# Performance work log

Hardware: AMD Instinct MI355X
Metric: run time of the kernel (lower is better)

The kernel has to match this reference:

```python
import jax, jax.numpy as jnp
import numpy as np

N, D = 8192, 32
SIGMA = 4.0
DAMPING = 0.5
MAX_ITER = 10
SHIFT_TOL = 1e-4


def _sqdist(a, b):
    # squared euclidean distances, (Na, Nb)
    sq = jnp.sum(a * a, axis=1)[:, None] + jnp.sum(b * b, axis=1)[None, :] - 2.0 * (a @ b.T)
    return jnp.maximum(sq, 0.0)


def setup_inputs() -> dict:
    key = jax.random.key(0)
    x = jax.random.normal(key, (N, D), dtype=jnp.float32)
    sigma = jnp.asarray(SIGMA, dtype=jnp.float32)  # learned scalar nn.Parameter
    return {"x": x, "sigma": sigma}


def _find_centroids(x, sigma):
    gamma = 1.0 / (2.0 * sigma ** 2)

    def body(carry, _):
        centroids, done = carry
        sq = _sqdist(x, centroids)              # (N, N); cdist(x,c)**2
        w = jnp.exp(-sq * gamma)                # gaussian kernel weights
        new_c = (w @ x) / jnp.sum(w, axis=1, keepdims=True)
        shift = jnp.linalg.norm(new_c - centroids, axis=1)
        # torch breaks BEFORE the damping update when max shift < tol
        done_new = done | (jnp.max(shift) < SHIFT_TOL)
        centroids = jnp.where(done_new, centroids,
                              DAMPING * centroids + (1.0 - DAMPING) * new_c)
        return (centroids, done_new), None

    (centroids, _), _ = jax.lax.scan(jax.remat(body), (x, jnp.asarray(False)), None, length=MAX_ITER)
    return centroids


def _nms_keep(x, centroids, threshold):
    n = centroids.shape[0]
    sq_pc = _sqdist(x, centroids)
    closest = jnp.argmin(sq_pc, axis=1)                      # (N,)
    scores = jnp.zeros((n,), jnp.int32).at[closest].add(1)   # counts per centroid
    sq_cc = _sqdist(centroids, centroids)
    overlap = (sq_cc < threshold ** 2) & ~jnp.eye(n, dtype=bool)
    order = jnp.argsort(-scores)                             # descending by score

    def body(keep, idx):
        active = keep[idx]
        keep2 = jnp.where(active, keep & ~overlap[idx], keep)
        keep2 = keep2.at[idx].set(jnp.where(active, scores[idx] > 0, keep2[idx]))
        return keep2, None

    keep, _ = jax.lax.scan(body, jnp.ones((n,), bool), order)
    return keep


def reference(x, sigma):
    centroids = _find_centroids(x, sigma)
    # threshold = sigma.item() in torch -> constant w.r.t. autodiff
    keep = _nms_keep(x, centroids, jax.lax.stop_gradient(sigma))
    # assignment over kept centroids only (dropped centroids get -inf cost -> 0 prob)
    cost = -jnp.sqrt(_sqdist(x, centroids) + 1e-12)
    cost = jnp.where(keep[None, :], cost, -jnp.inf)
    assignment = jax.nn.softmax(cost, axis=1)  # alpha == 1 branch
    return centroids, assignment, keep
```

## Files before the change

### kernel.cpp

```cpp
#include <hip/hip_runtime.h>
#include <math.h>

#define NPTS 8192
#define DIM 32
#define MAX_ITER 10
#define TOL 1e-4f
#define DAMP 0.5f
#define LOG2E 1.4426950408889634f

#define OFF_MSP   0u
#define OFF_CCUR  8650752u
#define OFF_CNEW  8912896u
#define OFF_NX    9175040u
#define OFF_NC    9183232u
#define OFF_PV    9191424u
#define OFF_PJ    9453568u
#define OFF_RKP   9715712u
#define OFF_MSH   9977856u
#define OFF_SCO   9977872u
#define OFF_ORD   9986064u

__global__ __launch_bounds__(256) void k_init(const float* __restrict__ x,
                                              float* __restrict__ c0,
                                              float* __restrict__ nx,
                                              float* __restrict__ nc,
                                              int* __restrict__ scores,
                                              unsigned int* __restrict__ msh) {
    int p = blockIdx.x * blockDim.x + threadIdx.x;
    const float4* xr = (const float4*)(x + (size_t)p * DIM);
    float4* cr = (float4*)(c0 + (size_t)p * DIM);
    float s = 0.f;
#pragma unroll
    for (int q = 0; q < 8; ++q) {
        float4 v = xr[q];
        cr[q] = v;
        s += v.x * v.x + v.y * v.y + v.z * v.z + v.w * v.w;
    }
    nx[p] = s;
    nc[p] = s;
    scores[p] = 0;
    if (blockIdx.x == 0 && threadIdx.x < 16) msh[threadIdx.x] = 0u;
}

__global__ __launch_bounds__(256, 2) void k_ms2(const float* __restrict__ x,
                                                const float* __restrict__ nx,
                                                const float* __restrict__ c,
                                                const float* __restrict__ nc,
                                                const float* __restrict__ sigma_p,
                                                float* __restrict__ P) {
    int t = threadIdx.x;
    int wv = __builtin_amdgcn_readfirstlane(t >> 6);
    int lane = t & 63;
    int it = (int)blockIdx.x >> 5, js = (int)blockIdx.x & 31;
    int i0 = it * 512 + wv * 128 + lane;
    int i1 = i0 + 64;

    float sg = sigma_p[0];
    float ng2 = -LOG2E / (2.f * sg * sg);

    float xi0[DIM], xi1[DIM];
    {
        const float4* xr0 = (const float4*)(x + (size_t)i0 * DIM);
        const float4* xr1 = (const float4*)(x + (size_t)i1 * DIM);
#pragma unroll
        for (int q = 0; q < 8; ++q) {
            float4 a = xr0[q], b = xr1[q];
            xi0[4 * q] = a.x; xi0[4 * q + 1] = a.y; xi0[4 * q + 2] = a.z; xi0[4 * q + 3] = a.w;
            xi1[4 * q] = b.x; xi1[4 * q + 1] = b.y; xi1[4 * q + 2] = b.z; xi1[4 * q + 3] = b.w;
        }
    }
    float nx0 = nx[i0], nx1 = nx[i1];

    float acc0[DIM], acc1[DIM];
#pragma unroll
    for (int d = 0; d < DIM; ++d) { acc0[d] = 0.f; acc1[d] = 0.f; }
    float ws0 = 0.f, ws1 = 0.f;

    int jb = js * 256;
    const float* cb = c + (size_t)jb * DIM;
    const float* xb = x + (size_t)jb * DIM;
    const float* ncb = nc + jb;

    for (int jj = 0; jj < 256; ++jj) {
        float w0, w1;
        {
            const float4* cr = (const float4*)(cb + (size_t)jj * DIM);
            float4 C[8];
#pragma unroll
            for (int q = 0; q < 8; ++q) C[q] = cr[q];
            float ncj = ncb[jj];
            float a0 = 0.f, a1 = 0.f, a2 = 0.f, a3 = 0.f;
            float b0 = 0.f, b1 = 0.f, b2 = 0.f, b3 = 0.f;
#pragma unroll
            for (int q = 0; q < 8; ++q) {
                a0 = fmaf(xi0[4 * q + 0], C[q].x, a0);
                a1 = fmaf(xi0[4 * q + 1], C[q].y, a1);
                a2 = fmaf(xi0[4 * q + 2], C[q].z, a2);
                a3 = fmaf(xi0[4 * q + 3], C[q].w, a3);
                b0 = fmaf(xi1[4 * q + 0], C[q].x, b0);
                b1 = fmaf(xi1[4 * q + 1], C[q].y, b1);
                b2 = fmaf(xi1[4 * q + 2], C[q].z, b2);
                b3 = fmaf(xi1[4 * q + 3], C[q].w, b3);
            }
            float sq0 = fmaxf(fmaf(-2.f, (a0 + a1) + (a2 + a3), nx0 + ncj), 0.f);
            float sq1 = fmaxf(fmaf(-2.f, (b0 + b1) + (b2 + b3), nx1 + ncj), 0.f);
            w0 = __builtin_amdgcn_exp2f(ng2 * sq0);
            w1 = __builtin_amdgcn_exp2f(ng2 * sq1);
        }
        ws0 += w0; ws1 += w1;
        {
            const float4* xr2 = (const float4*)(xb + (size_t)jj * DIM);
            float4 X[8];
#pragma unroll
            for (int q = 0; q < 8; ++q) X[q] = xr2[q];
#pragma unroll
            for (int q = 0; q < 8; ++q) {
                acc0[4 * q + 0] = fmaf(w0, X[q].x, acc0[4 * q + 0]);
                acc0[4 * q + 1] = fmaf(w0, X[q].y, acc0[4 * q + 1]);
                acc0[4 * q + 2] = fmaf(w0, X[q].z, acc0[4 * q + 2]);
                acc0[4 * q + 3] = fmaf(w0, X[q].w, acc0[4 * q + 3]);
                acc1[4 * q + 0] = fmaf(w1, X[q].x, acc1[4 * q + 0]);
                acc1[4 * q + 1] = fmaf(w1, X[q].y, acc1[4 * q + 1]);
                acc1[4 * q + 2] = fmaf(w1, X[q].z, acc1[4 * q + 2]);
                acc1[4 * q + 3] = fmaf(w1, X[q].w, acc1[4 * q + 3]);
            }
        }
    }

    size_t base = ((size_t)js * 33) * NPTS + i0;
#pragma unroll
    for (int d = 0; d < DIM; ++d) {
        P[base + (size_t)d * NPTS] = acc0[d];
        P[base + (size_t)d * NPTS + 64] = acc1[d];
    }
    P[base + (size_t)32 * NPTS] = ws0;
    P[base + (size_t)32 * NPTS + 64] = ws1;
}

__global__ __launch_bounds__(256) void k_reduce(const float* __restrict__ P,
                                                const float* __restrict__ c_cur,
                                                float* __restrict__ c_new,
                                                unsigned int* __restrict__ maxshift) {
    int i = blockIdx.x * 256 + threadIdx.x;
    float tot[33];
#pragma unroll
    for (int d = 0; d < 33; ++d) tot[d] = 0.f;
    for (int js = 0; js < 32; ++js) {
        size_t base = ((size_t)js * 33) * NPTS + i;
#pragma unroll
        for (int d = 0; d < 33; ++d) tot[d] += P[base + (size_t)d * NPTS];
    }
    float ws = tot[32];
    float inv = __builtin_amdgcn_rcpf(ws);
    inv = inv * (2.f - ws * inv);
    const float* co = c_cur + (size_t)i * DIM;
    float sh2 = 0.f;
    float ncv[DIM];
#pragma unroll
    for (int d = 0; d < DIM; ++d) {
        float v = tot[d] * inv;
        ncv[d] = v;
        float df = v - co[d];
        sh2 = fmaf(df, df, sh2);
    }
    float4* dst = (float4*)(c_new + (size_t)i * DIM);
#pragma unroll
    for (int q = 0; q < 8; ++q)
        dst[q] = make_float4(ncv[4 * q], ncv[4 * q + 1], ncv[4 * q + 2], ncv[4 * q + 3]);
    atomicMax(maxshift, __float_as_uint(__builtin_amdgcn_sqrtf(sh2)));
}

__global__ __launch_bounds__(256) void k_update(float* __restrict__ c_cur,
                                                const float* __restrict__ c_new,
                                                float* __restrict__ nc,
                                                const unsigned int* __restrict__ maxshift) {
    if (__uint_as_float(*maxshift) < TOL) return;
    int i = blockIdx.x * 256 + threadIdx.x;
    float4* cc = (float4*)(c_cur + (size_t)i * DIM);
    const float4* cn = (const float4*)(c_new + (size_t)i * DIM);
    float s = 0.f;
#pragma unroll
    for (int q = 0; q < 8; ++q) {
        float4 a = cc[q], b = cn[q];
        float4 r = make_float4(DAMP * a.x + (1.f - DAMP) * b.x,
                               DAMP * a.y + (1.f - DAMP) * b.y,
                               DAMP * a.z + (1.f - DAMP) * b.z,
                               DAMP * a.w + (1.f - DAMP) * b.w);
        cc[q] = r;
        s += r.x * r.x + r.y * r.y + r.z * r.z + r.w * r.w;
    }
    nc[i] = s;
}

__global__ __launch_bounds__(256, 2) void k_scores2(const float* __restrict__ x,
                                                    const float* __restrict__ nx,
                                                    const float* __restrict__ c,
                                                    const float* __restrict__ nc,
                                                    float* __restrict__ pv,
                                                    int* __restrict__ pj) {
    int t = threadIdx.x;
    int wv = __builtin_amdgcn_readfirstlane(t >> 6);
    int lane = t & 63;
    int it = (int)blockIdx.x >> 5, js = (int)blockIdx.x & 31;
    int p0 = it * 512 + wv * 128 + lane;
    int p1 = p0 + 64;

    float xi0[DIM], xi1[DIM];
    {
        const float4* xr0 = (const float4*)(x + (size_t)p0 * DIM);
        const float4* xr1 = (const float4*)(x + (size_t)p1 * DIM);
#pragma unroll
        for (int q = 0; q < 8; ++q) {
            float4 a = xr0[q], b = xr1[q];
            xi0[4 * q] = a.x; xi0[4 * q + 1] = a.y; xi0[4 * q + 2] = a.z; xi0[4 * q + 3] = a.w;
            xi1[4 * q] = b.x; xi1[4 * q + 1] = b.y; xi1[4 * q + 2] = b.z; xi1[4 * q + 3] = b.w;
        }
    }
    float nxp0 = nx[p0], nxp1 = nx[p1];

    int jb = js * 256;
    const float* cb = c + (size_t)jb * DIM;
    const float* ncb = nc + jb;
    float bv0 = INFINITY, bv1 = INFINITY;
    int bj0 = jb, bj1 = jb;
    for (int jj = 0; jj < 256; ++jj) {
        const float4* cr = (const float4*)(cb + (size_t)jj * DIM);
        float4 C[8];
#pragma unroll
        for (int q = 0; q < 8; ++q) C[q] = cr[q];
        float ncj = ncb[jj];
        float a0 = 0.f, a1 = 0.f, a2 = 0.f, a3 = 0.f;
        float b0 = 0.f, b1 = 0.f, b2 = 0.f, b3 = 0.f;
#pragma unroll
        for (int q = 0; q < 8; ++q) {
            a0 = fmaf(xi0[4 * q + 0], C[q].x, a0);
            a1 = fmaf(xi0[4 * q + 1], C[q].y, a1);
            a2 = fmaf(xi0[4 * q + 2], C[q].z, a2);
            a3 = fmaf(xi0[4 * q + 3], C[q].w, a3);
            b0 = fmaf(xi1[4 * q + 0], C[q].x, b0);
            b1 = fmaf(xi1[4 * q + 1], C[q].y, b1);
            b2 = fmaf(xi1[4 * q + 2], C[q].z, b2);
            b3 = fmaf(xi1[4 * q + 3], C[q].w, b3);
        }
        float sq0 = fmaxf(fmaf(-2.f, (a0 + a1) + (a2 + a3), nxp0 + ncj), 0.f);
        float sq1 = fmaxf(fmaf(-2.f, (b0 + b1) + (b2 + b3), nxp1 + ncj), 0.f);
        if (sq0 < bv0) { bv0 = sq0; bj0 = jb + jj; }
        if (sq1 < bv1) { bv1 = sq1; bj1 = jb + jj; }
    }
    pv[(size_t)js * NPTS + p0] = bv0;
    pj[(size_t)js * NPTS + p0] = bj0;
    pv[(size_t)js * NPTS + p1] = bv1;
    pj[(size_t)js * NPTS + p1] = bj1;
}

__global__ __launch_bounds__(256) void k_score_comb(const float* __restrict__ pv,
                                                    const int* __restrict__ pj,
                                                    int* __restrict__ scores) {
    int p = blockIdx.x * 256 + threadIdx.x;
    float bv = pv[p];
    int bj = pj[p];
    for (int js = 1; js < 32; ++js) {
        float v = pv[(size_t)js * NPTS + p];
        int j = pj[(size_t)js * NPTS + p];
        if (v < bv) { bv = v; bj = j; }
    }
    atomicAdd(&scores[bj], 1);
}

__global__ __launch_bounds__(256) void k_rank_part(const int* __restrict__ scores,
                                                   int* __restrict__ rkp) {
    int t = threadIdx.x;
    int wv = __builtin_amdgcn_readfirstlane(t >> 6);
    int lane = t & 63;
    int it = (int)blockIdx.x >> 5, js = (int)blockIdx.x & 31;
    int p = it * 256 + wv * 64 + lane;
    int sp = scores[p];
    int j0 = js * 256;
    int r = 0;
    for (int jj = 0; jj < 256; ++jj) {
        int sj = scores[j0 + jj];
        int j = j0 + jj;
        r += (sj > sp) || (sj == sp && j < p);
    }
    rkp[(size_t)js * NPTS + p] = r;
}

__global__ __launch_bounds__(256) void k_rank_comb(const int* __restrict__ rkp,
                                                   int* __restrict__ order) {
    int p = blockIdx.x * 256 + threadIdx.x;
    int r = 0;
    for (int js = 0; js < 32; ++js) r += rkp[(size_t)js * NPTS + p];
    order[r] = p;
}

__global__ __launch_bounds__(1024) void k_nms(const float* __restrict__ c,
                                              const int* __restrict__ order,
                                              const int* __restrict__ scores,
                                              const float* __restrict__ sigma_p,
                                              float* __restrict__ keep_out) {
    __shared__ int s_ord[NPTS];
    __shared__ unsigned char kp[NPTS];
    __shared__ int s_first[16];
    __shared__ int s_next;
    int t = threadIdx.x;
    for (int q = t; q < NPTS; q += 1024) { s_ord[q] = order[q]; kp[q] = 1; }
    __syncthreads();
    float sg = sigma_p[0];
    float thr2 = sg * sg;

    int k = 0;
    while (k < NPTS) {
        int cand = k + t;
        bool hit = (cand < NPTS) && (kp[s_ord[cand]] != 0);
        unsigned long long b = __ballot(hit);
        int wave = t >> 6;
        if ((t & 63) == 0)
            s_first[wave] = b ? (k + (wave << 6) + (__ffsll((unsigned long long)b) - 1))
                              : 0x7fffffff;
        __syncthreads();
        if (t == 0) {
            int mn = s_first[0];
            for (int w2 = 1; w2 < 16; ++w2) mn = min(mn, s_first[w2]);
            s_next = mn;
        }
        __syncthreads();
        int kf = s_next;
        if (kf == 0x7fffffff) { k += 1024; continue; }

        int idx = s_ord[kf];
        float ci[DIM];
        const float4* cr = (const float4*)(c + (size_t)idx * DIM);
#pragma unroll
        for (int q = 0; q < 8; ++q) {
            float4 v = cr[q];
            ci[4 * q] = v.x; ci[4 * q + 1] = v.y; ci[4 * q + 2] = v.z; ci[4 * q + 3] = v.w;
        }
#pragma unroll
        for (int m2 = 0; m2 < 8; ++m2) {
            int j = t + m2 * 1024;
            const float4* cj = (const float4*)(c + (size_t)j * DIM);
            float sq = 0.f;
#pragma unroll
            for (int q = 0; q < 8; ++q) {
                float4 v = cj[q];
                float e0 = v.x - ci[4 * q], e1 = v.y - ci[4 * q + 1];
                float e2 = v.z - ci[4 * q + 2], e3 = v.w - ci[4 * q + 3];
                sq += e0 * e0 + e1 * e1 + e2 * e2 + e3 * e3;
            }
            if (j != idx && sq < thr2) kp[j] = 0;
        }
        __syncthreads();
        if (t == 0) kp[idx] = (scores[idx] > 0) ? 1 : 0;
        __syncthreads();
        k = kf + 1;
    }
    __syncthreads();
    for (int q = t; q < NPTS; q += 1024) keep_out[q] = kp[q] ? 1.0f : 0.0f;
}

__global__ __launch_bounds__(256, 2) void k_apass1(const float* __restrict__ x,
                                                   const float* __restrict__ nx,
                                                   const float* __restrict__ c,
                                                   const float* __restrict__ nc,
                                                   const float* __restrict__ keepf,
                                                   float* __restrict__ ps) {
    int t = threadIdx.x;
    int wv = __builtin_amdgcn_readfirstlane(t >> 6);
    int lane = t & 63;
    int it = (int)blockIdx.x >> 5, js = (int)blockIdx.x & 31;
    int p0 = it * 512 + wv * 128 + lane;
    int p1 = p0 + 64;

    float xi0[DIM], xi1[DIM];
    {
        const float4* xr0 = (const float4*)(x + (size_t)p0 * DIM);
        const float4* xr1 = (const float4*)(x + (size_t)p1 * DIM);
#pragma unroll
        for (int q = 0; q < 8; ++q) {
            float4 a = xr0[q], b = xr1[q];
            xi0[4 * q] = a.x; xi0[4 * q + 1] = a.y; xi0[4 * q + 2] = a.z; xi0[4 * q + 3] = a.w;
            xi1[4 * q] = b.x; xi1[4 * q + 1] = b.y; xi1[4 * q + 2] = b.z; xi1[4 * q + 3] = b.w;
        }
    }
    float nxp0 = nx[p0], nxp1 = nx[p1];

    int jb = js * 256;
    const float* cb = c + (size_t)jb * DIM;
    const float* ncb = nc + jb;
    const float* kb = keepf + jb;
    float S0 = 0.f, S1 = 0.f;
    for (int jj = 0; jj < 256; ++jj) {
        const float4* cr = (const float4*)(cb + (size_t)jj * DIM);
        float4 C[8];
#pragma unroll
        for (int q = 0; q < 8; ++q) C[q] = cr[q];
        float ncj = ncb[jj];
        float kadd = (kb[jj] > 0.5f) ? 0.f : -1e38f;
        float a0 = 0.f, a1 = 0.f, a2 = 0.f, a3 = 0.f;
        float b0 = 0.f, b1 = 0.f, b2 = 0.f, b3 = 0.f;
#pragma unroll
        for (int q = 0; q < 8; ++q) {
            a0 = fmaf(xi0[4 * q + 0], C[q].x, a0);
            a1 = fmaf(xi0[4 * q + 1], C[q].y, a1);
            a2 = fmaf(xi0[4 * q + 2], C[q].z, a2);
            a3 = fmaf(xi0[4 * q + 3], C[q].w, a3);
            b0 = fmaf(xi1[4 * q + 0], C[q].x, b0);
            b1 = fmaf(xi1[4 * q + 1], C[q].y, b1);
            b2 = fmaf(xi1[4 * q + 2], C[q].z, b2);
            b3 = fmaf(xi1[4 * q + 3], C[q].w, b3);
        }
        float sq0 = fmaxf(fmaf(-2.f, (a0 + a1) + (a2 + a3), nxp0 + ncj), 0.f);
        float sq1 = fmaxf(fmaf(-2.f, (b0 + b1) + (b2 + b3), nxp1 + ncj), 0.f);
        float r0 = __builtin_amdgcn_sqrtf(sq0 + 1e-12f);
        float r1 = __builtin_amdgcn_sqrtf(sq1 + 1e-12f);
        S0 += __builtin_amdgcn_exp2f(fmaf(r0, -LOG2E, kadd));
        S1 += __builtin_amdgcn_exp2f(fmaf(r1, -LOG2E, kadd));
    }
    ps[(size_t)js * NPTS + p0] = S0;
    ps[(size_t)js * NPTS + p1] = S1;
}

__global__ __launch_bounds__(256, 4) void k_apass2(const float* __restrict__ x,
                                                   const float* __restrict__ c,
                                                   const float* __restrict__ keepf,
                                                   const float* __restrict__ ps,
                                                   float* __restrict__ A) {
    __shared__ float sx[128 * 36];
    __shared__ float snx[128];
    __shared__ float sscale[128];
    __shared__ float spart[256];
    int t = threadIdx.x;
    int wv = __builtin_amdgcn_readfirstlane(t >> 6);
    int lane = t & 63;
    int pt = (int)blockIdx.x >> 5, jt = (int)blockIdx.x & 31;
    int p0 = pt * 128, j0 = jt * 256;

    {
        const float4* src = (const float4*)(x + (size_t)p0 * DIM) + t * 4;
        int row = t >> 1, colh = (t & 1) * 16;
        float4* dst = (float4*)(sx + row * 36 + colh);
        float s = 0.f;
#pragma unroll
        for (int q = 0; q < 4; ++q) {
            float4 v = src[q];
            dst[q] = v;
            s += v.x * v.x + v.y * v.y + v.z * v.z + v.w * v.w;
        }
        spart[t] = s;
    }
    __syncthreads();
    if (t < 128) {
        snx[t] = spart[2 * t] + spart[2 * t + 1];
        float SS = 0.f;
        for (int js = 0; js < 32; ++js) SS += ps[(size_t)js * NPTS + p0 + t];
        sscale[t] = 1.f / SS;
    }

    int j = j0 + wv * 64 + lane;
    float cj[DIM];
    float ncj = 0.f;
    {
        const float4* cr = (const float4*)(c + (size_t)j * DIM);
#pragma unroll
        for (int q = 0; q < 8; ++q) {
            float4 v = cr[q];
            cj[4 * q] = v.x; cj[4 * q + 1] = v.y; cj[4 * q + 2] = v.z; cj[4 * q + 3] = v.w;
            ncj += v.x * v.x + v.y * v.y + v.z * v.z + v.w * v.w;
        }
    }
    float kadd = (keepf[j] > 0.5f) ? 0.f : -1e38f;
    __syncthreads();

    for (int pp = 0; pp < 128; ++pp) {
        const float4* xs = (const float4*)(sx + pp * 36);
        float d0 = 0.f, d1 = 0.f, d2 = 0.f, d3 = 0.f;
#pragma unroll
        for (int q = 0; q < 8; ++q) {
            float4 v = xs[q];
            d0 = fmaf(cj[4 * q + 0], v.x, d0);
            d1 = fmaf(cj[4 * q + 1], v.y, d1);
            d2 = fmaf(cj[4 * q + 2], v.z, d2);
            d3 = fmaf(cj[4 * q + 3], v.w, d3);
        }
        float sq = fmaxf(fmaf(-2.f, (d0 + d1) + (d2 + d3), snx[pp] + ncj), 0.f);
        float rt = __builtin_amdgcn_sqrtf(sq + 1e-12f);
        float tt = fmaf(rt, -LOG2E, kadd);
        A[(size_t)(p0 + pp) * NPTS + j] = __builtin_amdgcn_exp2f(tt) * sscale[pp];
    }
}

extern "C" void kernel_launch(void* const* d_in, const int* in_sizes, int n_in,
                              void* d_out, int out_size, void* d_ws, size_t ws_size,
                              hipStream_t stream) {
    const float* x = (const float*)d_in[0];
    const float* sigma = (const float*)d_in[1];

    float* out = (float*)d_out;
    float* OUT_C = out;
    float* A = out + (size_t)NPTS * DIM;
    float* OUT_K = A + (size_t)NPTS * NPTS;

    float* msP = A + OFF_MSP;
    float* c_cur = A + OFF_CCUR;
    float* c_new = A + OFF_CNEW;
    float* nx = A + OFF_NX;
    float* nc = A + OFF_NC;
    float* pv = A + OFF_PV;
    int* pj = (int*)(A + OFF_PJ);
    int* rkp = (int*)(A + OFF_RKP);
    unsigned int* msh = (unsigned int*)(A + OFF_MSH);
    int* scores = (int*)(A + OFF_SCO);
    int* order = (int*)(A + OFF_ORD);
    float* ps = (float*)d_ws;

    k_init<<<NPTS / 256, 256, 0, stream>>>(x, c_cur, nx, nc, scores, msh);
    for (int itr = 0; itr < MAX_ITER; ++itr) {
        k_ms2<<<512, 256, 0, stream>>>(x, nx, c_cur, nc, sigma, msP);
        k_reduce<<<NPTS / 256, 256, 0, stream>>>(msP, c_cur, c_new, msh + itr);
        k_update<<<NPTS / 256, 256, 0, stream>>>(c_cur, c_new, nc, msh + itr);
    }
    hipMemcpyAsync(OUT_C, c_cur, (size_t)NPTS * DIM * sizeof(float),
                   hipMemcpyDeviceToDevice, stream);

    k_scores2<<<512, 256, 0, stream>>>(x, nx, OUT_C, nc, pv, pj);
    k_score_comb<<<NPTS / 256, 256, 0, stream>>>(pv, pj, scores);
    k_rank_part<<<1024, 256, 0, stream>>>(scores, rkp);
    k_rank_comb<<<NPTS / 256, 256, 0, stream>>>(rkp, order);
    k_nms<<<1, 1024, 0, stream>>>(OUT_C, order, scores, sigma, OUT_K);

    k_apass1<<<512, 256, 0, stream>>>(x, nx, OUT_C, nc, OUT_K, ps);
    k_apass2<<<2048, 256, 0, stream>>>(x, OUT_C, OUT_K, ps, A);
}
```

Before: 1.822 ms.

## Double split-K partitions in mean-shift, scoring and softmax passes for more parallelism

Doubles the number of column splits in the mean-shift, argmin-score and softmax-sum kernels (512 to 1024 blocks), halving each block's inner loop and adding unroll-by-2. The reduce kernel now uses four waves per 64 points, each summing a quarter of the partials, and combines them through shared memory. Workspace offsets are shifted to fit the larger partial buffers. The softmax split count is chosen from the workspace size. The aim is better CU occupancy on the large GPU, at the cost of more partial-sum traffic and reduction work.

```diff
diff --git a/kernel.cpp b/kernel.cpp
--- a/kernel.cpp
+++ b/kernel.cpp
@@ -9,16 +9,16 @@
 #define LOG2E 1.4426950408889634f
 
 #define OFF_MSP   0u
-#define OFF_CCUR  8650752u
-#define OFF_CNEW  8912896u
-#define OFF_NX    9175040u
-#define OFF_NC    9183232u
-#define OFF_PV    9191424u
-#define OFF_PJ    9453568u
-#define OFF_RKP   9715712u
-#define OFF_MSH   9977856u
-#define OFF_SCO   9977872u
-#define OFF_ORD   9986064u
+#define OFF_CCUR  17301504u
+#define OFF_CNEW  17563648u
+#define OFF_NX    17825792u
+#define OFF_NC    17833984u
+#define OFF_PV    17842176u
+#define OFF_PJ    18366464u
+#define OFF_RKP   18890752u
+#define OFF_MSH   19152896u
+#define OFF_SCO   19152912u
+#define OFF_ORD   19161104u
 
 __global__ __launch_bounds__(256) void k_init(const float* __restrict__ x,
                                               float* __restrict__ c0,
@@ -51,7 +51,7 @@
     int t = threadIdx.x;
     int wv = __builtin_amdgcn_readfirstlane(t >> 6);
     int lane = t & 63;
-    int it = (int)blockIdx.x >> 5, js = (int)blockIdx.x & 31;
+    int it = (int)blockIdx.x >> 6, js = (int)blockIdx.x & 63;
     int i0 = it * 512 + wv * 128 + lane;
     int i1 = i0 + 64;
 
@@ -76,12 +76,13 @@
     for (int d = 0; d < DIM; ++d) { acc0[d] = 0.f; acc1[d] = 0.f; }
     float ws0 = 0.f, ws1 = 0.f;
 
-    int jb = js * 256;
+    int jb = js * 128;
     const float* cb = c + (size_t)jb * DIM;
     const float* xb = x + (size_t)jb * DIM;
     const float* ncb = nc + jb;
 
-    for (int jj = 0; jj < 256; ++jj) {
+#pragma unroll 2
+    for (int jj = 0; jj < 128; ++jj) {
         float w0, w1;
         {
             const float4* cr = (const float4*)(cb + (size_t)jj * DIM);
@@ -141,33 +142,46 @@
                                                 const float* __restrict__ c_cur,
                                                 float* __restrict__ c_new,
                                                 unsigned int* __restrict__ maxshift) {
-    int i = blockIdx.x * 256 + threadIdx.x;
+    __shared__ float red[256][33];
+    int t = threadIdx.x;
+    int pl = t & 63, qs = t >> 6;
+    int i = blockIdx.x * 64 + pl;
     float tot[33];
 #pragma unroll
     for (int d = 0; d < 33; ++d) tot[d] = 0.f;
-    for (int js = 0; js < 32; ++js) {
+    for (int js = qs * 16; js < qs * 16 + 16; ++js) {
         size_t base = ((size_t)js * 33) * NPTS + i;
 #pragma unroll
         for (int d = 0; d < 33; ++d) tot[d] += P[base + (size_t)d * NPTS];
     }
-    float ws = tot[32];
-    float inv = __builtin_amdgcn_rcpf(ws);
-    inv = inv * (2.f - ws * inv);
-    const float* co = c_cur + (size_t)i * DIM;
-    float sh2 = 0.f;
-    float ncv[DIM];
-#pragma unroll
-    for (int d = 0; d < DIM; ++d) {
-        float v = tot[d] * inv;
-        ncv[d] = v;
-        float df = v - co[d];
-        sh2 = fmaf(df, df, sh2);
-    }
-    float4* dst = (float4*)(c_new + (size_t)i * DIM);
-#pragma unroll
-    for (int q = 0; q < 8; ++q)
-        dst[q] = make_float4(ncv[4 * q], ncv[4 * q + 1], ncv[4 * q + 2], ncv[4 * q + 3]);
-    atomicMax(maxshift, __float_as_uint(__builtin_amdgcn_sqrtf(sh2)));
+#pragma unroll
+    for (int d = 0; d < 33; ++d) red[t][d] = tot[d];
+    __syncthreads();
+    if (t < 64) {
+        int ii = blockIdx.x * 64 + t;
+        float tt[33];
+#pragma unroll
+        for (int d = 0; d < 33; ++d)
+            tt[d] = (red[t][d] + red[t + 64][d]) + (red[t + 128][d] + red[t + 192][d]);
+        float ws = tt[32];
+        float inv = __builtin_amdgcn_rcpf(ws);
+        inv = inv * (2.f - ws * inv);
+        const float* co = c_cur + (size_t)ii * DIM;
+        float sh2 = 0.f;
+        float ncv[DIM];
+#pragma unroll
+        for (int d = 0; d < DIM; ++d) {
+            float v = tt[d] * inv;
+            ncv[d] = v;
+            float df = v - co[d];
+            sh2 = fmaf(df, df, sh2);
+        }
+        float4* dst = (float4*)(c_new + (size_t)ii * DIM);
+#pragma unroll
+        for (int q = 0; q < 8; ++q)
+            dst[q] = make_float4(ncv[4 * q], ncv[4 * q + 1], ncv[4 * q + 2], ncv[4 * q + 3]);
+        atomicMax(maxshift, __float_as_uint(__builtin_amdgcn_sqrtf(sh2)));
+    }
 }
 
 __global__ __launch_bounds__(256) void k_update(float* __restrict__ c_cur,
@@ -201,7 +215,7 @@
     int t = threadIdx.x;
     int wv = __builtin_amdgcn_readfirstlane(t >> 6);
     int lane = t & 63;
-    int it = (int)blockIdx.x >> 5, js = (int)blockIdx.x & 31;
+    int it = (int)blockIdx.x >> 6, js = (int)blockIdx.x & 63;
     int p0 = it * 512 + wv * 128 + lane;
     int p1 = p0 + 64;
 
@@ -218,12 +232,13 @@
     }
     float nxp0 = nx[p0], nxp1 = nx[p1];
 
-    int jb = js * 256;
+    int jb = js * 128;
     const float* cb = c + (size_t)jb * DIM;
     const float* ncb = nc + jb;
     float bv0 = INFINITY, bv1 = INFINITY;
     int bj0 = jb, bj1 = jb;
-    for (int jj = 0; jj < 256; ++jj) {
+#pragma unroll 2
+    for (int jj = 0; jj < 128; ++jj) {
         const float4* cr = (const float4*)(cb + (size_t)jj * DIM);
         float4 C[8];
 #pragma unroll
@@ -259,7 +274,7 @@
     int p = blockIdx.x * 256 + threadIdx.x;
     float bv = pv[p];
     int bj = pj[p];
-    for (int js = 1; js < 32; ++js) {
+    for (int js = 1; js < 64; ++js) {
         float v = pv[(size_t)js * NPTS + p];
         int j = pj[(size_t)js * NPTS + p];
         if (v < bv) { bv = v; bj = j; }
@@ -363,11 +378,14 @@
                                                    const float* __restrict__ c,
                                                    const float* __restrict__ nc,
                                                    const float* __restrict__ keepf,
-                                                   float* __restrict__ ps) {
+                                                   float* __restrict__ ps,
+                                                   int lsp) {
     int t = threadIdx.x;
     int wv = __builtin_amdgcn_readfirstlane(t >> 6);
     int lane = t & 63;
-    int it = (int)blockIdx.x >> 5, js = (int)blockIdx.x & 31;
+    int nsplit = 1 << lsp;
+    int it = (int)blockIdx.x >> lsp, js = (int)blockIdx.x & (nsplit - 1);
+    int jcount = NPTS >> lsp;
     int p0 = it * 512 + wv * 128 + lane;
     int p1 = p0 + 64;
 
@@ -384,12 +402,13 @@
     }
     float nxp0 = nx[p0], nxp1 = nx[p1];
 
-    int jb = js * 256;
+    int jb = js * jcount;
     const float* cb = c + (size_t)jb * DIM;
     const float* ncb = nc + jb;
     const float* kb = keepf + jb;
     float S0 = 0.f, S1 = 0.f;
-    for (int jj = 0; jj < 256; ++jj) {
+#pragma unroll 2
+    for (int jj = 0; jj < jcount; ++jj) {
         const float4* cr = (const float4*)(cb + (size_t)jj * DIM);
         float4 C[8];
 #pragma unroll
@@ -424,7 +443,8 @@
                                                    const float* __restrict__ c,
                                                    const float* __restrict__ keepf,
                                                    const float* __restrict__ ps,
-                                                   float* __restrict__ A) {
+                                                   float* __restrict__ A,
+                                                   int nsplit) {
     __shared__ float sx[128 * 36];
     __shared__ float snx[128];
     __shared__ float sscale[128];
@@ -452,7 +472,7 @@
     if (t < 128) {
         snx[t] = spart[2 * t] + spart[2 * t + 1];
         float SS = 0.f;
-        for (int js = 0; js < 32; ++js) SS += ps[(size_t)js * NPTS + p0 + t];
+        for (int js = 0; js < nsplit; ++js) SS += ps[(size_t)js * NPTS + p0 + t];
         sscale[t] = 1.f / SS;
     }
 
@@ -513,21 +533,23 @@
     int* order = (int*)(A + OFF_ORD);
     float* ps = (float*)d_ws;
 
+    int lsp = (ws_size >= (size_t)64 * NPTS * sizeof(float)) ? 6 : 5;
+
     k_init<<<NPTS / 256, 256, 0, stream>>>(x, c_cur, nx, nc, scores, msh);
     for (int itr = 0; itr < MAX_ITER; ++itr) {
-        k_ms2<<<512, 256, 0, stream>>>(x, nx, c_cur, nc, sigma, msP);
-        k_reduce<<<NPTS / 256, 256, 0, stream>>>(msP, c_cur, c_new, msh + itr);
+        k_ms2<<<1024, 256, 0, stream>>>(x, nx, c_cur, nc, sigma, msP);
+        k_reduce<<<NPTS / 64, 256, 0, stream>>>(msP, c_cur, c_new, msh + itr);
         k_update<<<NPTS / 256, 256, 0, stream>>>(c_cur, c_new, nc, msh + itr);
     }
     hipMemcpyAsync(OUT_C, c_cur, (size_t)NPTS * DIM * sizeof(float),
                    hipMemcpyDeviceToDevice, stream);
 
-    k_scores2<<<512, 256, 0, stream>>>(x, nx, OUT_C, nc, pv, pj);
+    k_scores2<<<1024, 256, 0, stream>>>(x, nx, OUT_C, nc, pv, pj);
     k_score_comb<<<NPTS / 256, 256, 0, stream>>>(pv, pj, scores);
     k_rank_part<<<1024, 256, 0, stream>>>(scores, rkp);
     k_rank_comb<<<NPTS / 256, 256, 0, stream>>>(rkp, order);
     k_nms<<<1, 1024, 0, stream>>>(OUT_C, order, scores, sigma, OUT_K);
 
-    k_apass1<<<512, 256, 0, stream>>>(x, nx, OUT_C, nc, OUT_K, ps);
-    k_apass2<<<2048, 256, 0, stream>>>(x, OUT_C, OUT_K, ps, A);
-}
+    k_apass1<<<16 << lsp, 256, 0, stream>>>(x, nx, OUT_C, nc, OUT_K, ps, lsp);
+    k_apass2<<<2048, 256, 0, stream>>>(x, OUT_C, OUT_K, ps, A, 1 << lsp);
+}
```

New measurement: 2.130 ms. 16.9% more time.

## Use constant address space scalar loads for wave-uniform rows and widen apass2 tile

Applied to the files above, without the earlier changes.

Wave-uniform centroid, x, norm and keep rows are now read through address_space(4) pointers as 16-wide vectors, so the compiler can issue scalar (SMEM) loads into SGPRs in place of per-lane vector loads. k_apass2 drops its LDS staging and reads x rows the same way. Each of its threads now computes two centroid columns, which halves the grid. The launch_bounds occupancy hints are removed, trading possible occupancy for register freedom. Scalar loads go through the scalar cache, so this relies on that path having enough bandwidth for the repeated row reads.

```diff
diff --git a/kernel.cpp b/kernel.cpp
--- a/kernel.cpp
+++ b/kernel.cpp
@@ -7,6 +7,16 @@
 #define TOL 1e-4f
 #define DAMP 0.5f
 #define LOG2E 1.4426950408889634f
+
+#define AS4 __attribute__((address_space(4)))
+typedef float f32x16 __attribute__((ext_vector_type(16)));
+
+__device__ __forceinline__ const AS4 float* cptr(const float* p) {
+    return (const AS4 float*)(unsigned long long)p;
+}
+__device__ __forceinline__ const AS4 int* cptri(const int* p) {
+    return (const AS4 int*)(unsigned long long)p;
+}
 
 #define OFF_MSP   0u
 #define OFF_CCUR  8650752u
@@ -42,18 +52,19 @@
     if (blockIdx.x == 0 && threadIdx.x < 16) msh[threadIdx.x] = 0u;
 }
 
-__global__ __launch_bounds__(256, 2) void k_ms2(const float* __restrict__ x,
-                                                const float* __restrict__ nx,
-                                                const float* __restrict__ c,
-                                                const float* __restrict__ nc,
-                                                const float* __restrict__ sigma_p,
-                                                float* __restrict__ P) {
+__global__ __launch_bounds__(256) void k_ms2(const float* __restrict__ x,
+                                             const float* __restrict__ nx,
+                                             const float* __restrict__ c,
+                                             const float* __restrict__ nc,
+                                             const float* __restrict__ sigma_p,
+                                             float* __restrict__ P) {
     int t = threadIdx.x;
     int wv = __builtin_amdgcn_readfirstlane(t >> 6);
     int lane = t & 63;
     int it = (int)blockIdx.x >> 5, js = (int)blockIdx.x & 31;
     int i0 = it * 512 + wv * 128 + lane;
     int i1 = i0 + 64;
+    int jb = js * 256;
 
     float sg = sigma_p[0];
     float ng2 = -LOG2E / (2.f * sg * sg);
@@ -76,31 +87,38 @@
     for (int d = 0; d < DIM; ++d) { acc0[d] = 0.f; acc1[d] = 0.f; }
     float ws0 = 0.f, ws1 = 0.f;
 
-    int jb = js * 256;
-    const float* cb = c + (size_t)jb * DIM;
-    const float* xb = x + (size_t)jb * DIM;
-    const float* ncb = nc + jb;
+    const AS4 f32x16* c16 = (const AS4 f32x16*)cptr(c + (size_t)jb * DIM);
+    const AS4 f32x16* x16 = (const AS4 f32x16*)cptr(x + (size_t)jb * DIM);
+    const AS4 float* nc4 = cptr(nc + jb);
 
     for (int jj = 0; jj < 256; ++jj) {
+        f32x16 C0 = c16[2 * jj], C1 = c16[2 * jj + 1];
+        float ncj = nc4[jj];
         float w0, w1;
         {
-            const float4* cr = (const float4*)(cb + (size_t)jj * DIM);
-            float4 C[8];
-#pragma unroll
-            for (int q = 0; q < 8; ++q) C[q] = cr[q];
-            float ncj = ncb[jj];
             float a0 = 0.f, a1 = 0.f, a2 = 0.f, a3 = 0.f;
             float b0 = 0.f, b1 = 0.f, b2 = 0.f, b3 = 0.f;
 #pragma unroll
-            for (int q = 0; q < 8; ++q) {
-                a0 = fmaf(xi0[4 * q + 0], C[q].x, a0);
-                a1 = fmaf(xi0[4 * q + 1], C[q].y, a1);
-                a2 = fmaf(xi0[4 * q + 2], C[q].z, a2);
-                a3 = fmaf(xi0[4 * q + 3], C[q].w, a3);
-                b0 = fmaf(xi1[4 * q + 0], C[q].x, b0);
-                b1 = fmaf(xi1[4 * q + 1], C[q].y, b1);
-                b2 = fmaf(xi1[4 * q + 2], C[q].z, b2);
-                b3 = fmaf(xi1[4 * q + 3], C[q].w, b3);
+            for (int q = 0; q < 4; ++q) {
+                a0 = fmaf(xi0[4 * q + 0], C0[4 * q + 0], a0);
+                a1 = fmaf(xi0[4 * q + 1], C0[4 * q + 1], a1);
+                a2 = fmaf(xi0[4 * q + 2], C0[4 * q + 2], a2);
+                a3 = fmaf(xi0[4 * q + 3], C0[4 * q + 3], a3);
+                b0 = fmaf(xi1[4 * q + 0], C0[4 * q + 0], b0);
+                b1 = fmaf(xi1[4 * q + 1], C0[4 * q + 1], b1);
+                b2 = fmaf(xi1[4 * q + 2], C0[4 * q + 2], b2);
+                b3 = fmaf(xi1[4 * q + 3], C0[4 * q + 3], b3);
+            }
+#pragma unroll
+            for (int q = 0; q < 4; ++q) {
+                a0 = fmaf(xi0[16 + 4 * q + 0], C1[4 * q + 0], a0);
+                a1 = fmaf(xi0[16 + 4 * q + 1], C1[4 * q + 1], a1);
+                a2 = fmaf(xi0[16 + 4 * q + 2], C1[4 * q + 2], a2);
+                a3 = fmaf(xi0[16 + 4 * q + 3], C1[4 * q + 3], a3);
+                b0 = fmaf(xi1[16 + 4 * q + 0], C1[4 * q + 0], b0);
+                b1 = fmaf(xi1[16 + 4 * q + 1], C1[4 * q + 1], b1);
+                b2 = fmaf(xi1[16 + 4 * q + 2], C1[4 * q + 2], b2);
+                b3 = fmaf(xi1[16 + 4 * q + 3], C1[4 * q + 3], b3);
             }
             float sq0 = fmaxf(fmaf(-2.f, (a0 + a1) + (a2 + a3), nx0 + ncj), 0.f);
             float sq1 = fmaxf(fmaf(-2.f, (b0 + b1) + (b2 + b3), nx1 + ncj), 0.f);
@@ -108,22 +126,16 @@
             w1 = __builtin_amdgcn_exp2f(ng2 * sq1);
         }
         ws0 += w0; ws1 += w1;
-        {
-            const float4* xr2 = (const float4*)(xb + (size_t)jj * DIM);
-            float4 X[8];
-#pragma unroll
-            for (int q = 0; q < 8; ++q) X[q] = xr2[q];
-#pragma unroll
-            for (int q = 0; q < 8; ++q) {
-                acc0[4 * q + 0] = fmaf(w0, X[q].x, acc0[4 * q + 0]);
-                acc0[4 * q + 1] = fmaf(w0, X[q].y, acc0[4 * q + 1]);
-                acc0[4 * q + 2] = fmaf(w0, X[q].z, acc0[4 * q + 2]);
-                acc0[4 * q + 3] = fmaf(w0, X[q].w, acc0[4 * q + 3]);
-                acc1[4 * q + 0] = fmaf(w1, X[q].x, acc1[4 * q + 0]);
-                acc1[4 * q + 1] = fmaf(w1, X[q].y, acc1[4 * q + 1]);
-                acc1[4 * q + 2] = fmaf(w1, X[q].z, acc1[4 * q + 2]);
-                acc1[4 * q + 3] = fmaf(w1, X[q].w, acc1[4 * q + 3]);
-            }
+        f32x16 X0 = x16[2 * jj], X1 = x16[2 * jj + 1];
+#pragma unroll
+        for (int e = 0; e < 16; ++e) {
+            acc0[e] = fmaf(w0, X0[e], acc0[e]);
+            acc1[e] = fmaf(w1, X0[e], acc1[e]);
+        }
+#pragma unroll
+        for (int e = 0; e < 16; ++e) {
+            acc0[16 + e] = fmaf(w0, X1[e], acc0[16 + e]);
+            acc1[16 + e] = fmaf(w1, X1[e], acc1[16 + e]);
         }
     }
 
@@ -192,18 +204,19 @@
     nc[i] = s;
 }
 
-__global__ __launch_bounds__(256, 2) void k_scores2(const float* __restrict__ x,
-                                                    const float* __restrict__ nx,
-                                                    const float* __restrict__ c,
-                                                    const float* __restrict__ nc,
-                                                    float* __restrict__ pv,
-                                                    int* __restrict__ pj) {
+__global__ __launch_bounds__(256) void k_scores2(const float* __restrict__ x,
+                                                 const float* __restrict__ nx,
+                                                 const float* __restrict__ c,
+                                                 const float* __restrict__ nc,
+                                                 float* __restrict__ pv,
+                                                 int* __restrict__ pj) {
     int t = threadIdx.x;
     int wv = __builtin_amdgcn_readfirstlane(t >> 6);
     int lane = t & 63;
     int it = (int)blockIdx.x >> 5, js = (int)blockIdx.x & 31;
     int p0 = it * 512 + wv * 128 + lane;
     int p1 = p0 + 64;
+    int jb = js * 256;
 
     float xi0[DIM], xi1[DIM];
     {
@@ -218,29 +231,37 @@
     }
     float nxp0 = nx[p0], nxp1 = nx[p1];
 
-    int jb = js * 256;
-    const float* cb = c + (size_t)jb * DIM;
-    const float* ncb = nc + jb;
+    const AS4 f32x16* c16 = (const AS4 f32x16*)cptr(c + (size_t)jb * DIM);
+    const AS4 float* nc4 = cptr(nc + jb);
+
     float bv0 = INFINITY, bv1 = INFINITY;
     int bj0 = jb, bj1 = jb;
     for (int jj = 0; jj < 256; ++jj) {
-        const float4* cr = (const float4*)(cb + (size_t)jj * DIM);
-        float4 C[8];
-#pragma unroll
-        for (int q = 0; q < 8; ++q) C[q] = cr[q];
-        float ncj = ncb[jj];
+        f32x16 C0 = c16[2 * jj], C1 = c16[2 * jj + 1];
+        float ncj = nc4[jj];
         float a0 = 0.f, a1 = 0.f, a2 = 0.f, a3 = 0.f;
         float b0 = 0.f, b1 = 0.f, b2 = 0.f, b3 = 0.f;
 #pragma unroll
-        for (int q = 0; q < 8; ++q) {
-            a0 = fmaf(xi0[4 * q + 0], C[q].x, a0);
-            a1 = fmaf(xi0[4 * q + 1], C[q].y, a1);
-            a2 = fmaf(xi0[4 * q + 2], C[q].z, a2);
-            a3 = fmaf(xi0[4 * q + 3], C[q].w, a3);
-            b0 = fmaf(xi1[4 * q + 0], C[q].x, b0);
-            b1 = fmaf(xi1[4 * q + 1], C[q].y, b1);
-            b2 = fmaf(xi1[4 * q + 2], C[q].z, b2);
-            b3 = fmaf(xi1[4 * q + 3], C[q].w, b3);
+        for (int q = 0; q < 4; ++q) {
+            a0 = fmaf(xi0[4 * q + 0], C0[4 * q + 0], a0);
+            a1 = fmaf(xi0[4 * q + 1], C0[4 * q + 1], a1);
+            a2 = fmaf(xi0[4 * q + 2], C0[4 * q + 2], a2);
+            a3 = fmaf(xi0[4 * q + 3], C0[4 * q + 3], a3);
+            b0 = fmaf(xi1[4 * q + 0], C0[4 * q + 0], b0);
+            b1 = fmaf(xi1[4 * q + 1], C0[4 * q + 1], b1);
+            b2 = fmaf(xi1[4 * q + 2], C0[4 * q + 2], b2);
+            b3 = fmaf(xi1[4 * q + 3], C0[4 * q + 3], b3);
+        }
+#pragma unroll
+        for (int q = 0; q < 4; ++q) {
+            a0 = fmaf(xi0[16 + 4 * q + 0], C1[4 * q + 0], a0);
+            a1 = fmaf(xi0[16 + 4 * q + 1], C1[4 * q + 1], a1);
+            a2 = fmaf(xi0[16 + 4 * q + 2], C1[4 * q + 2], a2);
+            a3 = fmaf(xi0[16 + 4 * q + 3], C1[4 * q + 3], a3);
+            b0 = fmaf(xi1[16 + 4 * q + 0], C1[4 * q + 0], b0);
+            b1 = fmaf(xi1[16 + 4 * q + 1], C1[4 * q + 1], b1);
+            b2 = fmaf(xi1[16 + 4 * q + 2], C1[4 * q + 2], b2);
+            b3 = fmaf(xi1[16 + 4 * q + 3], C1[4 * q + 3], b3);
         }
         float sq0 = fmaxf(fmaf(-2.f, (a0 + a1) + (a2 + a3), nxp0 + ncj), 0.f);
         float sq1 = fmaxf(fmaf(-2.f, (b0 + b1) + (b2 + b3), nxp1 + ncj), 0.f);
@@ -276,9 +297,10 @@
     int p = it * 256 + wv * 64 + lane;
     int sp = scores[p];
     int j0 = js * 256;
+    const AS4 int* sc4 = cptri(scores);
     int r = 0;
     for (int jj = 0; jj < 256; ++jj) {
-        int sj = scores[j0 + jj];
+        int sj = sc4[j0 + jj];
         int j = j0 + jj;
         r += (sj > sp) || (sj == sp && j < p);
     }
@@ -358,18 +380,19 @@
     for (int q = t; q < NPTS; q += 1024) keep_out[q] = kp[q] ? 1.0f : 0.0f;
 }
 
-__global__ __launch_bounds__(256, 2) void k_apass1(const float* __restrict__ x,
-                                                   const float* __restrict__ nx,
-                                                   const float* __restrict__ c,
-                                                   const float* __restrict__ nc,
-                                                   const float* __restrict__ keepf,
-                                                   float* __restrict__ ps) {
+__global__ __launch_bounds__(256) void k_apass1(const float* __restrict__ x,
+                                                const float* __restrict__ nx,
+                                                const float* __restrict__ c,
+                                                const float* __restrict__ nc,
+                                                const float* __restrict__ keepf,
+                                                float* __restrict__ ps) {
     int t = threadIdx.x;
     int wv = __builtin_amdgcn_readfirstlane(t >> 6);
     int lane = t & 63;
     int it = (int)blockIdx.x >> 5, js = (int)blockIdx.x & 31;
     int p0 = it * 512 + wv * 128 + lane;
     int p1 = p0 + 64;
+    int jb = js * 256;
 
     float xi0[DIM], xi1[DIM];
     {
@@ -384,30 +407,38 @@
     }
     float nxp0 = nx[p0], nxp1 = nx[p1];
 
-    int jb = js * 256;
-    const float* cb = c + (size_t)jb * DIM;
-    const float* ncb = nc + jb;
-    const float* kb = keepf + jb;
+    const AS4 f32x16* c16 = (const AS4 f32x16*)cptr(c + (size_t)jb * DIM);
+    const AS4 float* nc4 = cptr(nc + jb);
+    const AS4 float* kp4 = cptr(keepf + jb);
+
     float S0 = 0.f, S1 = 0.f;
     for (int jj = 0; jj < 256; ++jj) {
-        const float4* cr = (const float4*)(cb + (size_t)jj * DIM);
-        float4 C[8];
-#pragma unroll
-        for (int q = 0; q < 8; ++q) C[q] = cr[q];
-        float ncj = ncb[jj];
-        float kadd = (kb[jj] > 0.5f) ? 0.f : -1e38f;
+        f32x16 C0 = c16[2 * jj], C1 = c16[2 * jj + 1];
+        float ncj = nc4[jj];
+        float kadd = (kp4[jj] > 0.5f) ? 0.f : -1e38f;
         float a0 = 0.f, a1 = 0.f, a2 = 0.f, a3 = 0.f;
         float b0 = 0.f, b1 = 0.f, b2 = 0.f, b3 = 0.f;
 #pragma unroll
-        for (int q = 0; q < 8; ++q) {
-            a0 = fmaf(xi0[4 * q + 0], C[q].x, a0);
-            a1 = fmaf(xi0[4 * q + 1], C[q].y, a1);
-            a2 = fmaf(xi0[4 * q + 2], C[q].z, a2);
-            a3 = fmaf(xi0[4 * q + 3], C[q].w, a3);
-            b0 = fmaf(xi1[4 * q + 0], C[q].x, b0);
-            b1 = fmaf(xi1[4 * q + 1], C[q].y, b1);
-            b2 = fmaf(xi1[4 * q + 2], C[q].z, b2);
-            b3 = fmaf(xi1[4 * q + 3], C[q].w, b3);
+        for (int q = 0; q < 4; ++q) {
+            a0 = fmaf(xi0[4 * q + 0], C0[4 * q + 0], a0);
+            a1 = fmaf(xi0[4 * q + 1], C0[4 * q + 1], a1);
+            a2 = fmaf(xi0[4 * q + 2], C0[4 * q + 2], a2);
+            a3 = fmaf(xi0[4 * q + 3], C0[4 * q + 3], a3);
+            b0 = fmaf(xi1[4 * q + 0], C0[4 * q + 0], b0);
+            b1 = fmaf(xi1[4 * q + 1], C0[4 * q + 1], b1);
+            b2 = fmaf(xi1[4 * q + 2], C0[4 * q + 2], b2);
+            b3 = fmaf(xi1[4 * q + 3], C0[4 * q + 3], b3);
+        }
+#pragma unroll
+        for (int q = 0; q < 4; ++q) {
+            a0 = fmaf(xi0[16 + 4 * q + 0], C1[4 * q + 0], a0);
+            a1 = fmaf(xi0[16 + 4 * q + 1], C1[4 * q + 1], a1);
+            a2 = fmaf(xi0[16 + 4 * q + 2], C1[4 * q + 2], a2);
+            a3 = fmaf(xi0[16 + 4 * q + 3], C1[4 * q + 3], a3);
+            b0 = fmaf(xi1[16 + 4 * q + 0], C1[4 * q + 0], b0);
+            b1 = fmaf(xi1[16 + 4 * q + 1], C1[4 * q + 1], b1);
+            b2 = fmaf(xi1[16 + 4 * q + 2], C1[4 * q + 2], b2);
+            b3 = fmaf(xi1[16 + 4 * q + 3], C1[4 * q + 3], b3);
         }
         float sq0 = fmaxf(fmaf(-2.f, (a0 + a1) + (a2 + a3), nxp0 + ncj), 0.f);
         float sq1 = fmaxf(fmaf(-2.f, (b0 + b1) + (b2 + b3), nxp1 + ncj), 0.f);
@@ -420,72 +451,91 @@
     ps[(size_t)js * NPTS + p1] = S1;
 }
 
-__global__ __launch_bounds__(256, 4) void k_apass2(const float* __restrict__ x,
-                                                   const float* __restrict__ c,
-                                                   const float* __restrict__ keepf,
-                                                   const float* __restrict__ ps,
-                                                   float* __restrict__ A) {
-    __shared__ float sx[128 * 36];
+__global__ __launch_bounds__(256) void k_apass2(const float* __restrict__ x,
+                                                const float* __restrict__ c,
+                                                const float* __restrict__ keepf,
+                                                const float* __restrict__ ps,
+                                                float* __restrict__ A) {
     __shared__ float snx[128];
     __shared__ float sscale[128];
-    __shared__ float spart[256];
     int t = threadIdx.x;
     int wv = __builtin_amdgcn_readfirstlane(t >> 6);
     int lane = t & 63;
-    int pt = (int)blockIdx.x >> 5, jt = (int)blockIdx.x & 31;
-    int p0 = pt * 128, j0 = jt * 256;
-
-    {
-        const float4* src = (const float4*)(x + (size_t)p0 * DIM) + t * 4;
-        int row = t >> 1, colh = (t & 1) * 16;
-        float4* dst = (float4*)(sx + row * 36 + colh);
+    int pt = (int)blockIdx.x >> 4, jt = (int)blockIdx.x & 15;
+    int p0 = pt * 128, j0 = jt * 512;
+
+    if (t < 128) {
+        const float4* xr = (const float4*)(x + (size_t)(p0 + t) * DIM);
         float s = 0.f;
 #pragma unroll
-        for (int q = 0; q < 4; ++q) {
-            float4 v = src[q];
-            dst[q] = v;
+        for (int q = 0; q < 8; ++q) {
+            float4 v = xr[q];
             s += v.x * v.x + v.y * v.y + v.z * v.z + v.w * v.w;
         }
-        spart[t] = s;
-    }
-    __syncthreads();
-    if (t < 128) {
-        snx[t] = spart[2 * t] + spart[2 * t + 1];
+        snx[t] = s;
         float SS = 0.f;
         for (int js = 0; js < 32; ++js) SS += ps[(size_t)js * NPTS + p0 + t];
         sscale[t] = 1.f / SS;
     }
 
-    int j = j0 + wv * 64 + lane;
-    float cj[DIM];
-    float ncj = 0.f;
+    int ja = j0 + wv * 64 + lane;
+    int jbx = ja + 256;
+    float cj0[DIM], cj1[DIM];
+    float nc0 = 0.f, nc1 = 0.f;
     {
-        const float4* cr = (const float4*)(c + (size_t)j * DIM);
+        const float4* cra = (const float4*)(c + (size_t)ja * DIM);
+        const float4* crb = (const float4*)(c + (size_t)jbx * DIM);
 #pragma unroll
         for (int q = 0; q < 8; ++q) {
-            float4 v = cr[q];
-            cj[4 * q] = v.x; cj[4 * q + 1] = v.y; cj[4 * q + 2] = v.z; cj[4 * q + 3] = v.w;
-            ncj += v.x * v.x + v.y * v.y + v.z * v.z + v.w * v.w;
-        }
-    }
-    float kadd = (keepf[j] > 0.5f) ? 0.f : -1e38f;
+            float4 va = cra[q], vb = crb[q];
+            cj0[4 * q] = va.x; cj0[4 * q + 1] = va.y; cj0[4 * q + 2] = va.z; cj0[4 * q + 3] = va.w;
+            cj1[4 * q] = vb.x; cj1[4 * q + 1] = vb.y; cj1[4 * q + 2] = vb.z; cj1[4 * q + 3] = vb.w;
+            nc0 += va.x * va.x + va.y * va.y + va.z * va.z + va.w * va.w;
+            nc1 += vb.x * vb.x + vb.y * vb.y + vb.z * vb.z + vb.w * vb.w;
+        }
+    }
+    float kadd0 = (keepf[ja] > 0.5f) ? 0.f : -1e38f;
+    float kadd1 = (keepf[jbx] > 0.5f) ? 0.f : -1e38f;
     __syncthreads();
 
+    const AS4 f32x16* x16 = (const AS4 f32x16*)cptr(x + (size_t)p0 * DIM);
+
     for (int pp = 0; pp < 128; ++pp) {
-        const float4* xs = (const float4*)(sx + pp * 36);
+        f32x16 X0 = x16[2 * pp], X1 = x16[2 * pp + 1];
         float d0 = 0.f, d1 = 0.f, d2 = 0.f, d3 = 0.f;
-#pragma unroll
-        for (int q = 0; q < 8; ++q) {
-            float4 v = xs[q];
-            d0 = fmaf(cj[4 * q + 0], v.x, d0);
-            d1 = fmaf(cj[4 * q + 1], v.y, d1);
-            d2 = fmaf(cj[4 * q + 2], v.z, d2);
-            d3 = fmaf(cj[4 * q + 3], v.w, d3);
-        }
-        float sq = fmaxf(fmaf(-2.f, (d0 + d1) + (d2 + d3), snx[pp] + ncj), 0.f);
-        float rt = __builtin_amdgcn_sqrtf(sq + 1e-12f);
-        float tt = fmaf(rt, -LOG2E, kadd);
-        A[(size_t)(p0 + pp) * NPTS + j] = __builtin_amdgcn_exp2f(tt) * sscale[pp];
+        float e0 = 0.f, e1 = 0.f, e2 = 0.f, e3 = 0.f;
+#pragma unroll
+        for (int q = 0; q < 4; ++q) {
+            d0 = fmaf(cj0[4 * q + 0], X0[4 * q + 0], d0);
+            d1 = fmaf(cj0[4 * q + 1], X0[4 * q + 1], d1);
+            d2 = fmaf(cj0[4 * q + 2], X0[4 * q + 2], d2);
+            d3 = fmaf(cj0[4 * q + 3], X0[4 * q + 3], d3);
+            e0 = fmaf(cj1[4 * q + 0], X0[4 * q + 0], e0);
+            e1 = fmaf(cj1[4 * q + 1], X0[4 * q + 1], e1);
+            e2 = fmaf(cj1[4 * q + 2], X0[4 * q + 2], e2);
+            e3 = fmaf(cj1[4 * q + 3], X0[4 * q + 3], e3);
+        }
+#pragma unroll
+        for (int q = 0; q < 4; ++q) {
+            d0 = fmaf(cj0[16 + 4 * q + 0], X1[4 * q + 0], d0);
+            d1 = fmaf(cj0[16 + 4 * q + 1], X1[4 * q + 1], d1);
+            d2 = fmaf(cj0[16 + 4 * q + 2], X1[4 * q + 2], d2);
+            d3 = fmaf(cj0[16 + 4 * q + 3], X1[4 * q + 3], d3);
+            e0 = fmaf(cj1[16 + 4 * q + 0], X1[4 * q + 0], e0);
+            e1 = fmaf(cj1[16 + 4 * q + 1], X1[4 * q + 1], e1);
+            e2 = fmaf(cj1[16 + 4 * q + 2], X1[4 * q + 2], e2);
+            e3 = fmaf(cj1[16 + 4 * q + 3], X1[4 * q + 3], e3);
+        }
+        float nxp = snx[pp], scl = sscale[pp];
+        float sqa = fmaxf(fmaf(-2.f, (d0 + d1) + (d2 + d3), nxp + nc0), 0.f);
+        float sqb = fmaxf(fmaf(-2.f, (e0 + e1) + (e2 + e3), nxp + nc1), 0.f);
+        float ra = __builtin_amdgcn_sqrtf(sqa + 1e-12f);
+        float rb = __builtin_amdgcn_sqrtf(sqb + 1e-12f);
+        float ta = fmaf(ra, -LOG2E, kadd0);
+        float tb = fmaf(rb, -LOG2E, kadd1);
+        float* rowp = A + (size_t)(p0 + pp) * NPTS;
+        rowp[ja] = __builtin_amdgcn_exp2f(ta) * scl;
+        rowp[jbx] = __builtin_amdgcn_exp2f(tb) * scl;
     }
 }
 
@@ -529,5 +579,5 @@
     k_nms<<<1, 1024, 0, stream>>>(OUT_C, order, scores, sigma, OUT_K);
 
     k_apass1<<<512, 256, 0, stream>>>(x, nx, OUT_C, nc, OUT_K, ps);
-    k_apass2<<<2048, 256, 0, stream>>>(x, OUT_C, OUT_K, ps, A);
-}
+    k_apass2<<<1024, 256, 0, stream>>>(x, OUT_C, OUT_K, ps, A);
+}
```

New measurement: 1.883 ms. 3.3% more time.
